# Kernel tuning notes

Measured on AMD Instinct MI355X. Metric: run time of the kernel, lower is better.

## Reference

```python
import jax, jax.numpy as jnp
import numpy as np

B, C, H, W = 4, 192, 128, 128
K = 2048            # selected (changed) tokens per image
HEADS = 3
HD = C // HEADS     # 64
HID = 4 * C         # 768, ConvMlp hidden
N = H * W
EPS = 1e-5


def _layernorm(x, w, b):
    mu = jnp.mean(x, axis=-1, keepdims=True)
    var = jnp.mean((x - mu) ** 2, axis=-1, keepdims=True)
    return (x - mu) / jnp.sqrt(var + EPS) * w + b


def setup_inputs() -> dict:
    key = jax.random.key(0)
    ks = jax.random.split(key, 12)
    x = jax.random.normal(ks[0], (B, C, H, W), dtype=jnp.float32)
    # unique sorted indices per batch (scatter-back must be well defined)
    pkeys = jax.random.split(ks[1], B)
    indices = jnp.sort(
        jax.vmap(lambda k: jax.random.permutation(k, N)[:K])(pkeys), axis=-1
    ).astype(jnp.int64)
    s = 0.02
    return {
        "x": x,
        "indices": indices,
        "ln1_w": jnp.ones((C,), jnp.float32),
        "ln1_b": jnp.zeros((C,), jnp.float32),
        "qkv_w": jax.random.normal(ks[2], (3 * C, C), jnp.float32) * s,
        "proj_w": jax.random.normal(ks[3], (C, C), jnp.float32) * s,
        "proj_b": jnp.zeros((C,), jnp.float32),
        "ln2_w": jnp.ones((C,), jnp.float32),
        "ln2_b": jnp.zeros((C,), jnp.float32),
        "fc1_w": jax.random.normal(ks[4], (HID, C), jnp.float32) * s,
        "fc1_b": jnp.zeros((HID,), jnp.float32),
        "dw_w": jax.random.normal(ks[5], (HID, 1, 3, 3), jnp.float32) * s,  # depthwise OIHW
        "fc2_w": jax.random.normal(ks[6], (C, HID), jnp.float32) * s,
        "fc2_b": jnp.zeros((C,), jnp.float32),
    }


def reference(x, indices, ln1_w, ln1_b, qkv_w, proj_w, proj_b,
              ln2_w, ln2_b, fc1_w, fc1_b, dw_w, fc2_w, fc2_b):
    scale = HD ** (-0.5)
    tokens = x.reshape(B, C, N).transpose(0, 2, 1)          # b n c
    y = _layernorm(tokens, ln1_w, ln1_b)

    # --- masked_attn: gather -> dense MHA on subset -> scatter back ---
    br = jnp.arange(B)[:, None]
    sel = y[br, indices]                                    # b k c
    qkv = sel @ qkv_w.T                                     # b k 3c (no bias)
    qkv = qkv.reshape(B, K, 3, HEADS, HD).transpose(2, 0, 3, 1, 4)
    q, k, v = qkv[0], qkv[1], qkv[2]                        # b h k d
    attn = jax.nn.softmax(jnp.einsum("bhqd,bhkd->bhqk", q, k) * scale, axis=-1)
    out = jnp.einsum("bhqk,bhkd->bhqd", attn, v)            # b h k d
    out = out.transpose(0, 2, 1, 3).reshape(B, K, C) @ proj_w.T + proj_b
    y = y.at[br, indices].set(out)

    tokens = tokens + y                                     # residual adds norm1(x) w/ attn-updated subset
    tokens = _layernorm(tokens, ln2_w, ln2_b)

    # --- ConvMlp: fc1 -> depthwise 3x3 -> GELU -> fc2 ---
    h1 = tokens @ fc1_w.T + fc1_b                           # b n hid
    img = h1.transpose(0, 2, 1).reshape(B, HID, H, W)
    img = jax.lax.conv_general_dilated(
        img, dw_w, (1, 1), "SAME",
        dimension_numbers=("NCHW", "OIHW", "NCHW"),
        feature_group_count=HID)
    h1 = img.reshape(B, HID, N).transpose(0, 2, 1)
    h1 = jax.nn.gelu(h1, approximate=False)
    h2 = h1 @ fc2_w.T + fc2_b

    tokens = tokens + h2
    return tokens.transpose(0, 2, 1).reshape(B, C, H, W)
```

## Files before the change

kernel.cpp:

```cpp
#include <hip/hip_runtime.h>

#define B_ 4
#define C_ 192
#define H_ 128
#define W_ 128
#define N_ (H_*W_)
#define K_ 2048
#define HEADS_ 3
#define HD_ 64
#define HID_ 768
#define NC_ 8
#define KC_ (K_/NC_)

typedef __attribute__((ext_vector_type(4))) float f32x4;
typedef __attribute__((ext_vector_type(8))) short bf16x8;

__device__ __forceinline__ unsigned short f2bf(float f){
  unsigned int u = __float_as_uint(f);
  u += 0x7FFFu + ((u >> 16) & 1u);
  return (unsigned short)(u >> 16);
}
__device__ __forceinline__ float bf2f(unsigned short s){
  return __uint_as_float(((unsigned int)s) << 16);
}
__device__ __forceinline__ unsigned cvtpk(float lo, float hi){
  unsigned r;
  asm("v_cvt_pk_bf16_f32 %0, %1, %2" : "=v"(r) : "v"(lo), "v"(hi));
  return r;
}

__device__ __forceinline__ int load_idx(const unsigned* __restrict__ ip, int pos){
  bool is64 = (ip[1]==0u) & (ip[3]==0u) & (ip[5]==0u) & (ip[7]==0u);
  int v = is64 ? (int)ip[2*pos] : (int)ip[pos];
  return min(max(v, 0), N_-1);
}

__global__ __launch_bounds__(256) void k_ln1(const float* __restrict__ x,
    const float* __restrict__ w, const float* __restrict__ bias,
    unsigned short* __restrict__ y, int b_off){
  int blk = blockIdx.x;
  int bl = blk >> 8;
  int b  = b_off + bl;
  int n0 = (blk & 255) * 64;
  int t  = threadIdx.x;
  int tok = t & 63, q = t >> 6;
  __shared__ float tile[64][C_+1];
  __shared__ float red[8][64];
  __shared__ float wls[C_], bls[C_];
  if (t < C_){ wls[t] = w[t]; bls[t] = bias[t]; }
  const float* xb = x + (size_t)b*C_*N_ + n0;
  float sum = 0.f, sq = 0.f;
#pragma unroll
  for (int i = 0; i < 48; ++i){
    int c = q + 4*i;
    float v = xb[(size_t)c*N_ + tok];
    tile[tok][c] = v;
    sum += v; sq += v*v;
  }
  red[q][tok] = sum; red[4+q][tok] = sq;
  __syncthreads();
  if (q == 0){
    float s  = red[0][tok]+red[1][tok]+red[2][tok]+red[3][tok];
    float s2 = red[4][tok]+red[5][tok]+red[6][tok]+red[7][tok];
    float mu = s*(1.f/C_);
    float rstd = rsqrtf(s2*(1.f/C_) - mu*mu + 1e-5f);
    red[0][tok] = mu; red[1][tok] = rstd;
  }
  __syncthreads();
  unsigned* yb = reinterpret_cast<unsigned*>(y + ((size_t)bl*N_ + n0)*C_);
#pragma unroll
  for (int i = 0; i < 24; ++i){
    int li = t + 256*i;
    int tk = li / 96, c2 = li % 96;
    int c = 2*c2;
    float v0 = (tile[tk][c]  -red[0][tk])*red[1][tk]*wls[c]   + bls[c];
    float v1 = (tile[tk][c+1]-red[0][tk])*red[1][tk]*wls[c+1] + bls[c+1];
    yb[li] = (unsigned)f2bf(v0) | ((unsigned)f2bf(v1) << 16);
  }
}

__global__ __launch_bounds__(256) void k_qkv(const unsigned short* __restrict__ y,
    const unsigned* __restrict__ idx, const float* __restrict__ wq,
    unsigned short* __restrict__ qkv, int b_off){
  const int NT = (3*C_)/64;
  int bid = blockIdx.x;
  int bl  = bid / (16*NT);
  int rem = bid % (16*NT);
  int m0  = (rem / NT) * 128;
  int n0  = (rem % NT) * 64;
  int t = threadIdx.x, lane = t & 63;
  int wv = t >> 6, wm = wv & 1, wn = wv >> 1;
  __shared__ unsigned short Al[128][40];
  __shared__ unsigned short Bl[64][40];
  __shared__ int rows[128];
  if (t < 128) rows[t] = load_idx(idx, (b_off+bl)*K_ + m0 + t);
  __syncthreads();
  f32x4 acc[4][2] = {};
  int l15 = lane & 15, lhi = lane >> 4;
  for (int k0 = 0; k0 < C_; k0 += 32){
    {
      int m = t >> 1;
      const unsigned short* src = y + ((size_t)bl*N_ + rows[m])*C_ + k0;
#pragma unroll
      for (int i = 0; i < 4; ++i){
        int kq = (t & 1) + 2*i;
        *reinterpret_cast<ushort4*>(&Al[m][4*kq]) =
            *reinterpret_cast<const ushort4*>(src + 4*kq);
      }
      int n = t >> 2;
      const float* bsrc = wq + (size_t)(n0+n)*C_ + k0;
#pragma unroll
      for (int i = 0; i < 2; ++i){
        int q = (t & 3) + 4*i;
        float4 v = *reinterpret_cast<const float4*>(bsrc + 4*q);
        ushort4 p; p.x=f2bf(v.x); p.y=f2bf(v.y); p.z=f2bf(v.z); p.w=f2bf(v.w);
        *reinterpret_cast<ushort4*>(&Bl[n][4*q]) = p;
      }
    }
    __syncthreads();
    bf16x8 af[4], bfr[2];
#pragma unroll
    for (int mf = 0; mf < 4; ++mf)
      af[mf] = *reinterpret_cast<const bf16x8*>(&Al[wm*64 + mf*16 + l15][lhi*8]);
#pragma unroll
    for (int nf = 0; nf < 2; ++nf)
      bfr[nf] = *reinterpret_cast<const bf16x8*>(&Bl[wn*32 + nf*16 + l15][lhi*8]);
#pragma unroll
    for (int mf = 0; mf < 4; ++mf)
#pragma unroll
      for (int nf = 0; nf < 2; ++nf)
        acc[mf][nf] = __builtin_amdgcn_mfma_f32_16x16x32_bf16(af[mf], bfr[nf], acc[mf][nf], 0,0,0);
    __syncthreads();
  }
#pragma unroll
  for (int mf = 0; mf < 4; ++mf){
    int mb = m0 + wm*64 + mf*16 + lhi*4;
#pragma unroll
    for (int nf = 0; nf < 2; ++nf){
      int n = n0 + wn*32 + nf*16 + l15;
#pragma unroll
      for (int r = 0; r < 4; ++r)
        qkv[((size_t)bl*K_ + mb + r)*(3*C_) + n] = f2bf(acc[mf][nf][r]);
    }
  }
}

__global__ __launch_bounds__(256) void k_attn(const unsigned short* __restrict__ qkv,
    float* __restrict__ po, float* __restrict__ pml, int nb){
  int bid = blockIdx.x;
  int c   = bid & (NC_-1);
  int qt  = (bid >> 3) & 31;
  int bh  = bid >> 8;
  int h = bh % HEADS_, bl = bh / HEADS_;
  int q0 = qt*64;
  int t = threadIdx.x, lane = t & 63, wv = t >> 6;
  int l15 = lane & 15, lhi = lane >> 4;
  const unsigned short* base = qkv + (size_t)bl*K_*(3*C_) + h*HD_;
  __shared__ unsigned short Ql[64][72];
  __shared__ unsigned short Kl[64][72];
  __shared__ unsigned short Vt[64][72];
  __shared__ unsigned short Pl[4][16][72];
  {
    int r = t >> 2, d0 = (t & 3) * 16;
    const uint4* src = reinterpret_cast<const uint4*>(base + (size_t)(q0+r)*(3*C_) + d0);
    *reinterpret_cast<uint4*>(&Ql[r][d0])   = src[0];
    *reinterpret_cast<uint4*>(&Ql[r][d0+8]) = src[1];
  }
  __syncthreads();
  float m_q = -1e30f, l_q = 0.f;
  f32x4 o[4] = {};
  for (int kt0 = c*KC_; kt0 < c*KC_ + KC_; kt0 += 64){
    {
      int r = t >> 2, d0 = (t & 3) * 16;
      const uint4* src = reinterpret_cast<const uint4*>(base + (size_t)(kt0+r)*(3*C_) + C_ + d0);
      *reinterpret_cast<uint4*>(&Kl[r][d0])   = src[0];
      *reinterpret_cast<uint4*>(&Kl[r][d0+8]) = src[1];
      int kp = t & 31, vd0 = (t >> 5) * 8, k = 2*kp;
      const ushort4* v0 = reinterpret_cast<const ushort4*>(base + (size_t)(kt0+k)*(3*C_)   + 2*C_ + vd0);
      const ushort4* v1 = reinterpret_cast<const ushort4*>(base + (size_t)(kt0+k+1)*(3*C_) + 2*C_ + vd0);
      ushort4 a0 = v0[0], a1 = v0[1], b0 = v1[0], b1 = v1[1];
      unsigned short va[8] = {a0.x,a0.y,a0.z,a0.w,a1.x,a1.y,a1.z,a1.w};
      unsigned short vb[8] = {b0.x,b0.y,b0.z,b0.w,b1.x,b1.y,b1.z,b1.w};
#pragma unroll
      for (int j = 0; j < 8; ++j){
        unsigned u = (unsigned)va[j] | ((unsigned)vb[j] << 16);
        *reinterpret_cast<unsigned*>(&Vt[vd0+j][k]) = u;
      }
    }
    __syncthreads();
    f32x4 s[4] = {};
    __builtin_amdgcn_s_setprio(1);
#pragma unroll
    for (int kt = 0; kt < 2; ++kt){
      bf16x8 qf = *reinterpret_cast<const bf16x8*>(&Ql[wv*16 + l15][kt*32 + lhi*8]);
#pragma unroll
      for (int nt = 0; nt < 4; ++nt){
        bf16x8 kf = *reinterpret_cast<const bf16x8*>(&Kl[nt*16 + l15][kt*32 + lhi*8]);
        s[nt] = __builtin_amdgcn_mfma_f32_16x16x32_bf16(kf, qf, s[nt], 0,0,0);
      }
    }
    __builtin_amdgcn_s_setprio(0);
    float mx = s[0][0];
#pragma unroll
    for (int nt = 0; nt < 4; ++nt)
#pragma unroll
      for (int reg = 0; reg < 4; ++reg) mx = fmaxf(mx, s[nt][reg]);
    mx = fmaxf(mx, __shfl_xor(mx, 16));
    mx = fmaxf(mx, __shfl_xor(mx, 32));
    mx *= 0.125f;
    bool skip = __all(mx <= m_q + 8.f);
    if (!skip){
      float mn = fmaxf(m_q, mx);
      float corr = __expf(m_q - mn);
      l_q *= corr;
      float cr[4];
#pragma unroll
      for (int reg = 0; reg < 4; ++reg) cr[reg] = __shfl(corr, lhi*4 + reg);
#pragma unroll
      for (int nt = 0; nt < 4; ++nt)
#pragma unroll
        for (int reg = 0; reg < 4; ++reg) o[nt][reg] *= cr[reg];
      m_q = mn;
    }
    float ls = 0.f;
#pragma unroll
    for (int nt = 0; nt < 4; ++nt){
      float p0 = __expf(fmaf(s[nt][0], 0.125f, -m_q));
      float p1 = __expf(fmaf(s[nt][1], 0.125f, -m_q));
      float p2 = __expf(fmaf(s[nt][2], 0.125f, -m_q));
      float p3 = __expf(fmaf(s[nt][3], 0.125f, -m_q));
      ls += (p0 + p1) + (p2 + p3);
      uint2 uu;
      uu.x = cvtpk(p0, p1);
      uu.y = cvtpk(p2, p3);
      *reinterpret_cast<uint2*>(&Pl[wv][l15][nt*16 + lhi*4]) = uu;
    }
    ls += __shfl_xor(ls, 16);
    ls += __shfl_xor(ls, 32);
    l_q += ls;
    __threadfence_block();
    __builtin_amdgcn_s_setprio(1);
#pragma unroll
    for (int kt = 0; kt < 2; ++kt){
      bf16x8 pa = *reinterpret_cast<const bf16x8*>(&Pl[wv][l15][kt*32 + lhi*8]);
#pragma unroll
      for (int nt = 0; nt < 4; ++nt){
        bf16x8 vb = *reinterpret_cast<const bf16x8*>(&Vt[nt*16 + l15][kt*32 + lhi*8]);
        o[nt] = __builtin_amdgcn_mfma_f32_16x16x32_bf16(pa, vb, o[nt], 0,0,0);
      }
    }
    __builtin_amdgcn_s_setprio(0);
    __syncthreads();
  }
  int R = nb*HEADS_*K_;
  int rowb = (bl*HEADS_ + h)*K_;
#pragma unroll
  for (int reg = 0; reg < 4; ++reg){
    int rq = rowb + q0 + wv*16 + lhi*4 + reg;
#pragma unroll
    for (int nt = 0; nt < 4; ++nt)
      po[((size_t)c*R + rq)*HD_ + nt*16 + l15] = o[nt][reg];
  }
  if (lhi == 0){
    int rq = rowb + q0 + wv*16 + l15;
    *reinterpret_cast<float2*>(pml + 2*((size_t)c*R + rq)) = make_float2(m_q, l_q);
  }
}

__global__ __launch_bounds__(256) void k_amerge(const float* __restrict__ po,
    const float* __restrict__ pml, unsigned short* __restrict__ ao, int nb){
  int R = nb*HEADS_*K_;
  int row = blockIdx.x*4 + (threadIdx.x >> 6);
  int lane = threadIdx.x & 63;
  float m[NC_], l[NC_];
#pragma unroll
  for (int cc = 0; cc < NC_; ++cc){
    float2 v = *reinterpret_cast<const float2*>(pml + 2*((size_t)cc*R + row));
    m[cc] = v.x; l[cc] = v.y;
  }
  float M = m[0];
#pragma unroll
  for (int cc = 1; cc < NC_; ++cc) M = fmaxf(M, m[cc]);
  float L = 0.f, o = 0.f;
#pragma unroll
  for (int cc = 0; cc < NC_; ++cc){
    float e = __expf(m[cc] - M);
    L += l[cc]*e;
    o += e * po[((size_t)cc*R + row)*HD_ + lane];
  }
  o /= L;
  int q = row & (K_-1);
  int bh = row >> 11;
  int h = bh % HEADS_, bl = bh / HEADS_;
  ao[((size_t)bl*K_ + q)*C_ + h*HD_ + lane] = f2bf(o);
}

__global__ __launch_bounds__(256) void k_proj(const unsigned short* __restrict__ ain,
    const unsigned* __restrict__ idx, const float* __restrict__ pw,
    const float* __restrict__ pb, unsigned short* __restrict__ y, int b_off){
  const int NT = C_/64;
  int bid = blockIdx.x;
  int bl  = bid / (16*NT);
  int rem = bid % (16*NT);
  int m0  = (rem / NT) * 128;
  int n0  = (rem % NT) * 64;
  int t = threadIdx.x, lane = t & 63;
  int wv = t >> 6, wm = wv & 1, wn = wv >> 1;
  __shared__ unsigned short Al[128][40];
  __shared__ unsigned short Bl[64][40];
  __shared__ int rows[128];
  if (t < 128) rows[t] = load_idx(idx, (b_off+bl)*K_ + m0 + t);
  __syncthreads();
  f32x4 acc[4][2] = {};
  int l15 = lane & 15, lhi = lane >> 4;
  for (int k0 = 0; k0 < C_; k0 += 32){
    {
      int m = t >> 1;
      const unsigned short* src = ain + ((size_t)bl*K_ + m0 + m)*C_ + k0;
#pragma unroll
      for (int i = 0; i < 4; ++i){
        int kq = (t & 1) + 2*i;
        *reinterpret_cast<ushort4*>(&Al[m][4*kq]) =
            *reinterpret_cast<const ushort4*>(src + 4*kq);
      }
      int n = t >> 2;
      const float* bsrc = pw + (size_t)(n0+n)*C_ + k0;
#pragma unroll
      for (int i = 0; i < 2; ++i){
        int q = (t & 3) + 4*i;
        float4 v = *reinterpret_cast<const float4*>(bsrc + 4*q);
        ushort4 p; p.x=f2bf(v.x); p.y=f2bf(v.y); p.z=f2bf(v.z); p.w=f2bf(v.w);
        *reinterpret_cast<ushort4*>(&Bl[n][4*q]) = p;
      }
    }
    __syncthreads();
    bf16x8 af[4], bfr[2];
#pragma unroll
    for (int mf = 0; mf < 4; ++mf)
      af[mf] = *reinterpret_cast<const bf16x8*>(&Al[wm*64 + mf*16 + l15][lhi*8]);
#pragma unroll
    for (int nf = 0; nf < 2; ++nf)
      bfr[nf] = *reinterpret_cast<const bf16x8*>(&Bl[wn*32 + nf*16 + l15][lhi*8]);
#pragma unroll
    for (int mf = 0; mf < 4; ++mf)
#pragma unroll
      for (int nf = 0; nf < 2; ++nf)
        acc[mf][nf] = __builtin_amdgcn_mfma_f32_16x16x32_bf16(af[mf], bfr[nf], acc[mf][nf], 0,0,0);
    __syncthreads();
  }
#pragma unroll
  for (int mf = 0; mf < 4; ++mf){
    int mb = wm*64 + mf*16 + lhi*4;
#pragma unroll
    for (int nf = 0; nf < 2; ++nf){
      int n = n0 + wn*32 + nf*16 + l15;
      float bv = pb[n];
#pragma unroll
      for (int r = 0; r < 4; ++r)
        y[((size_t)bl*N_ + rows[mb + r])*C_ + n] = f2bf(acc[mf][nf][r] + bv);
    }
  }
}

__global__ __launch_bounds__(256) void k_ln2(const float* __restrict__ x,
    const unsigned short* __restrict__ y, const float* __restrict__ w,
    const float* __restrict__ bias, float* __restrict__ ln2t, int b_off){
  int blk = blockIdx.x;
  int bl = blk >> 8;
  int b  = b_off + bl;
  int n0 = (blk & 255) * 64;
  int t  = threadIdx.x;
  int tok = t & 63, q = t >> 6;
  __shared__ float tile[64][C_+1];
  __shared__ float red[8][64];
  __shared__ float wls[C_], bls[C_];
  if (t < C_){ wls[t] = w[t]; bls[t] = bias[t]; }
  const unsigned* yb = reinterpret_cast<const unsigned*>(y + ((size_t)bl*N_ + n0)*C_);
#pragma unroll
  for (int i = 0; i < 24; ++i){
    int li = t + 256*i;
    unsigned u = yb[li];
    int tk = li / 96, c2 = li % 96;
    tile[tk][2*c2]   = bf2f((unsigned short)(u & 0xffffu));
    tile[tk][2*c2+1] = bf2f((unsigned short)(u >> 16));
  }
  __syncthreads();
  const float* xb = x + (size_t)b*C_*N_ + n0;
  float sum = 0.f, sq = 0.f;
#pragma unroll
  for (int i = 0; i < 48; ++i){
    int c = q + 4*i;
    float v = xb[(size_t)c*N_ + tok] + tile[tok][c];
    tile[tok][c] = v;
    sum += v; sq += v*v;
  }
  red[q][tok] = sum; red[4+q][tok] = sq;
  __syncthreads();
  if (q == 0){
    float s  = red[0][tok]+red[1][tok]+red[2][tok]+red[3][tok];
    float s2 = red[4][tok]+red[5][tok]+red[6][tok]+red[7][tok];
    float mu = s*(1.f/C_);
    float rstd = rsqrtf(s2*(1.f/C_) - mu*mu + 1e-5f);
    red[0][tok] = mu; red[1][tok] = rstd;
  }
  __syncthreads();
  float* ob = ln2t + (size_t)b*C_*N_ + n0;
  float mu = red[0][tok], rstd = red[1][tok];
#pragma unroll
  for (int i = 0; i < 48; ++i){
    int c = q + 4*i;
    ob[(size_t)c*N_ + tok] = (tile[tok][c]-mu)*rstd*wls[c] + bls[c];
  }
}

__global__ __launch_bounds__(256) void k_fc1(const float* __restrict__ ln2t,
    const float* __restrict__ wgt, const float* __restrict__ bias,
    unsigned short* __restrict__ h1, int b_off){
  int bid = blockIdx.x;
  int bl  = bid >> 8;
  int rem = bid & 255;
  int m0  = (rem >> 1) * 128;
  int nh  = (rem & 1) * 6;
  int t = threadIdx.x, lane = t & 63;
  int wv = t >> 6, wm = wv & 1, wn = wv >> 1;
  int l15 = lane & 15, lhi = lane >> 4;
  __shared__ unsigned short Al[128][200];
  __shared__ unsigned short Bl[64][200];
  const float* a = ln2t + (size_t)(b_off+bl)*C_*N_ + m0;
  unsigned short* hb = h1 + (size_t)bl*HID_*N_;
  {
    int m = t & 127, half = t >> 7;
#pragma unroll
    for (int i = 0; i < 48; ++i){
      int p = half + 2*i;
      float v0 = a[(size_t)(2*p)*N_ + m];
      float v1 = a[(size_t)(2*p+1)*N_ + m];
      unsigned u = (unsigned)f2bf(v0) | ((unsigned)f2bf(v1) << 16);
      *reinterpret_cast<unsigned*>(&Al[m][2*p]) = u;
    }
  }
  for (int nt = 0; nt < 6; ++nt){
    int n0 = (nh + nt)*64;
    __syncthreads();
    {
      int n = t >> 2;
      const float* bsrc = wgt + (size_t)(n0+n)*C_;
#pragma unroll
      for (int i = 0; i < 12; ++i){
        int q = (t & 3) + 4*i;
        float4 v = *reinterpret_cast<const float4*>(bsrc + 4*q);
        ushort4 p; p.x=f2bf(v.x); p.y=f2bf(v.y); p.z=f2bf(v.z); p.w=f2bf(v.w);
        *reinterpret_cast<ushort4*>(&Bl[n][4*q]) = p;
      }
    }
    __syncthreads();
    f32x4 acc[4][2] = {};
#pragma unroll
    for (int ks = 0; ks < 6; ++ks){
      bf16x8 af[4], bfr[2];
#pragma unroll
      for (int mf = 0; mf < 4; ++mf)
        af[mf] = *reinterpret_cast<const bf16x8*>(&Al[wm*64 + mf*16 + l15][ks*32 + lhi*8]);
#pragma unroll
      for (int nf = 0; nf < 2; ++nf)
        bfr[nf] = *reinterpret_cast<const bf16x8*>(&Bl[wn*32 + nf*16 + l15][ks*32 + lhi*8]);
#pragma unroll
      for (int mf = 0; mf < 4; ++mf)
#pragma unroll
        for (int nf = 0; nf < 2; ++nf)
          acc[mf][nf] = __builtin_amdgcn_mfma_f32_16x16x32_bf16(af[mf], bfr[nf], acc[mf][nf], 0,0,0);
    }
#pragma unroll
    for (int mf = 0; mf < 4; ++mf){
      int mb = m0 + wm*64 + mf*16 + lhi*4;
#pragma unroll
      for (int nf = 0; nf < 2; ++nf){
        int n = n0 + wn*32 + nf*16 + l15;
        float bv = bias[n];
        ushort4 pk;
        pk.x = f2bf(acc[mf][nf][0] + bv);
        pk.y = f2bf(acc[mf][nf][1] + bv);
        pk.z = f2bf(acc[mf][nf][2] + bv);
        pk.w = f2bf(acc[mf][nf][3] + bv);
        *reinterpret_cast<ushort4*>(&hb[(size_t)n*N_ + mb]) = pk;
      }
    }
  }
}

__global__ __launch_bounds__(512) void k_fc2f(const unsigned short* __restrict__ h1,
    const float* __restrict__ dw, const float* __restrict__ wgt,
    const float* __restrict__ bias, float* __restrict__ out, int b_off){
  int nwg = gridDim.x;
  int cpx = nwg >> 3;
  int bid = (blockIdx.x & 7)*cpx + (blockIdx.x >> 3);
  int bl  = bid >> 7;
  int r   = bid & 127;
  int b   = b_off + bl;
  int t = threadIdx.x, lane = t & 63, wv = t >> 6;
  int wm = wv & 1, wn = wv >> 1;
  int l15 = lane & 15, lhi = lane >> 4;
  __shared__ unsigned short Ht[32][3][136];
  __shared__ unsigned short Alc[128][40];
  __shared__ unsigned short Bl[192][40];
  __shared__ float Dwl[288];
  const unsigned short* h1b = h1 + (size_t)bl*HID_*N_;
  f32x4 acc[4][3] = {};
  int cch = t & 31, j0 = (t >> 5) * 8;
  for (int k0 = 0; k0 < HID_; k0 += 32){
    __syncthreads();
#pragma unroll
    for (int i = 0; i < 3; ++i){
      int li = t + 512*i;
      int ch = li / 48, rem = li % 48, dy = rem >> 4, seg = rem & 15;
      int rr = r - 1 + dy;
      uint4 v = make_uint4(0u,0u,0u,0u);
      if (rr >= 0 && rr < H_)
        v = *reinterpret_cast<const uint4*>(h1b + (size_t)(k0+ch)*N_ + rr*W_ + seg*8);
      *reinterpret_cast<uint4*>(&Ht[ch][dy][seg*8]) = v;
    }
#pragma unroll
    for (int i = 0; i < 3; ++i){
      int li = t + 512*i;
      int row = li >> 3, seg = li & 7;
      float4 v = *reinterpret_cast<const float4*>(wgt + (size_t)row*HID_ + k0 + seg*4);
      ushort4 p; p.x=f2bf(v.x); p.y=f2bf(v.y); p.z=f2bf(v.z); p.w=f2bf(v.w);
      *reinterpret_cast<ushort4*>(&Bl[row][seg*4]) = p;
    }
    if (t < 288) Dwl[t] = dw[k0*9 + t];
    __syncthreads();
    {
      const float* wp = &Dwl[cch*9];
      float s[8] = {0.f,0.f,0.f,0.f,0.f,0.f,0.f,0.f};
#pragma unroll
      for (int dy = 0; dy < 3; ++dy){
        const unsigned short* rp = &Ht[cch][dy][j0];
        bf16x8 mid = *reinterpret_cast<const bf16x8*>(rp);
        float v[10];
        v[0] = (j0 > 0)   ? bf2f(rp[-1]) : 0.f;
        v[9] = (j0 < 120) ? bf2f(rp[8])  : 0.f;
#pragma unroll
        for (int j = 0; j < 8; ++j) v[1+j] = bf2f((unsigned short)mid[j]);
        float wa = wp[3*dy], wb = wp[3*dy+1], wc = wp[3*dy+2];
#pragma unroll
        for (int j = 0; j < 8; ++j)
          s[j] += v[j]*wa + v[j+1]*wb + v[j+2]*wc;
      }
#pragma unroll
      for (int j = 0; j < 8; ++j){
        float xx = s[j];
        Alc[j0+j][cch] = f2bf(0.5f*xx*(1.f + erff(xx*0.70710678f)));
      }
    }
    __syncthreads();
    bf16x8 af[4], bfr[3];
#pragma unroll
    for (int mf = 0; mf < 4; ++mf)
      af[mf] = *reinterpret_cast<const bf16x8*>(&Alc[wm*64 + mf*16 + l15][lhi*8]);
#pragma unroll
    for (int nf = 0; nf < 3; ++nf)
      bfr[nf] = *reinterpret_cast<const bf16x8*>(&Bl[wn*48 + nf*16 + l15][lhi*8]);
    __builtin_amdgcn_s_setprio(1);
#pragma unroll
    for (int mf = 0; mf < 4; ++mf)
#pragma unroll
      for (int nf = 0; nf < 3; ++nf)
        acc[mf][nf] = __builtin_amdgcn_mfma_f32_16x16x32_bf16(af[mf], bfr[nf], acc[mf][nf], 0,0,0);
    __builtin_amdgcn_s_setprio(0);
  }
#pragma unroll
  for (int mf = 0; mf < 4; ++mf){
    int tok = r*W_ + wm*64 + mf*16 + lhi*4;
#pragma unroll
    for (int nf = 0; nf < 3; ++nf){
      int oc = wn*48 + nf*16 + l15;
      float bv = bias[oc];
      size_t off = ((size_t)b*C_ + oc)*N_ + tok;
      float4 rr = *reinterpret_cast<const float4*>(out + off);
      float4 v = make_float4(rr.x + acc[mf][nf][0] + bv, rr.y + acc[mf][nf][1] + bv,
                             rr.z + acc[mf][nf][2] + bv, rr.w + acc[mf][nf][3] + bv);
      *reinterpret_cast<float4*>(out + off) = v;
    }
  }
}

extern "C" void kernel_launch(void* const* d_in, const int* in_sizes, int n_in,
                              void* d_out, int out_size, void* d_ws, size_t ws_size,
                              hipStream_t stream) {
  const float*    x      = (const float*)d_in[0];
  const unsigned* idx    = (const unsigned*)d_in[1];
  const float*    ln1_w  = (const float*)d_in[2];
  const float*    ln1_b  = (const float*)d_in[3];
  const float*    qkv_w  = (const float*)d_in[4];
  const float*    proj_w = (const float*)d_in[5];
  const float*    proj_b = (const float*)d_in[6];
  const float*    ln2_w  = (const float*)d_in[7];
  const float*    ln2_b  = (const float*)d_in[8];
  const float*    fc1_w  = (const float*)d_in[9];
  const float*    fc1_b  = (const float*)d_in[10];
  const float*    dw_w   = (const float*)d_in[11];
  const float*    fc2_w  = (const float*)d_in[12];
  const float*    fc2_b  = (const float*)d_in[13];
  float* out = (float*)d_out;

  const size_t SZY = (size_t)N_*C_*2;
  const size_t SZQ = (size_t)K_*3*C_*2;
  const size_t SZA = (size_t)K_*C_*2;
  const size_t SZO = (size_t)NC_*HEADS_*K_*HD_*4;
  const size_t SZH = (size_t)HID_*N_*2;
  int nb = (ws_size >= (size_t)B_*SZH) ? B_ : 1;

  char* ws = (char*)d_ws;
  unsigned short* y16  = (unsigned short*)ws;
  unsigned short* qkvb = (unsigned short*)(ws + (size_t)nb*SZY);
  unsigned short* aob  = (unsigned short*)(ws + (size_t)nb*(SZY+SZQ));
  float*          po   = (float*)(ws + (size_t)nb*(SZY+SZQ+SZA));
  float*          pml  = (float*)(ws + (size_t)nb*(SZY+SZQ+SZA+SZO));
  unsigned short* h1s  = (unsigned short*)ws;

  for (int b0 = 0; b0 < B_; b0 += nb){
    k_ln1   <<<nb*256,             256, 0, stream>>>(x, ln1_w, ln1_b, y16, b0);
    k_qkv   <<<nb*16*9,            256, 0, stream>>>(y16, idx, qkv_w, qkvb, b0);
    k_attn  <<<nb*HEADS_*32*NC_,   256, 0, stream>>>(qkvb, po, pml, nb);
    k_amerge<<<nb*HEADS_*K_/4,     256, 0, stream>>>(po, pml, aob, nb);
    k_proj  <<<nb*16*3,            256, 0, stream>>>(aob, idx, proj_w, proj_b, y16, b0);
    k_ln2   <<<nb*256,             256, 0, stream>>>(x, y16, ln2_w, ln2_b, out, b0);
    k_fc1   <<<nb*256,             256, 0, stream>>>(out, fc1_w, fc1_b, h1s, b0);
    k_fc2f  <<<nb*128,             512, 0, stream>>>(h1s, dw_w, fc2_w, fc2_b, out, b0);
  }
}
```

Before: 269.8 us.

## Split fc2 tiles into half-row blocks and use tanh GELU approximation

The fused depthwise-conv/GELU/fc2 kernel now handles half an image row (64 tokens) per workgroup instead of a full row. This doubles the grid and raises occupancy, and the shared-memory tile is reorganised with halo columns. The exact erf GELU is replaced with a tanh-based approximation built on __expf to cut transcendental cost. The trade-offs are more redundant halo loads, fc2 weight tiles loaded twice as often, and a small numerical deviation from exact GELU.

```diff
diff --git a/kernel.cpp b/kernel.cpp
--- a/kernel.cpp
+++ b/kernel.cpp
@@ -27,6 +27,13 @@
   unsigned r;
   asm("v_cvt_pk_bf16_f32 %0, %1, %2" : "=v"(r) : "v"(lo), "v"(hi));
   return r;
+}
+__device__ __forceinline__ float gelu_fast(float x){
+  float y = 0.7978845608f*x*(1.f + 0.044715f*x*x);
+  float e = __expf(2.f*fabsf(y));
+  float t = 1.f - 2.f/(1.f + e);
+  t = copysignf(t, y);
+  return 0.5f*x*(1.f + t);
 }
 
 __device__ __forceinline__ int load_idx(const unsigned* __restrict__ ip, int pos){
@@ -494,30 +501,35 @@
   int nwg = gridDim.x;
   int cpx = nwg >> 3;
   int bid = (blockIdx.x & 7)*cpx + (blockIdx.x >> 3);
-  int bl  = bid >> 7;
-  int r   = bid & 127;
+  int bl  = bid >> 8;
+  int rem = bid & 255;
+  int r    = rem >> 1;
+  int c0   = (rem & 1) * 64;
   int b   = b_off + bl;
   int t = threadIdx.x, lane = t & 63, wv = t >> 6;
   int wm = wv & 1, wn = wv >> 1;
   int l15 = lane & 15, lhi = lane >> 4;
-  __shared__ unsigned short Ht[32][3][136];
-  __shared__ unsigned short Alc[128][40];
+  __shared__ unsigned short Ht[3][32][88];
+  __shared__ unsigned short Alc[64][48];
   __shared__ unsigned short Bl[192][40];
   __shared__ float Dwl[288];
   const unsigned short* h1b = h1 + (size_t)bl*HID_*N_;
-  f32x4 acc[4][3] = {};
-  int cch = t & 31, j0 = (t >> 5) * 8;
+  f32x4 acc[2][3] = {};
+  int cch = t & 31, grp = t >> 5;
   for (int k0 = 0; k0 < HID_; k0 += 32){
     __syncthreads();
 #pragma unroll
-    for (int i = 0; i < 3; ++i){
+    for (int i = 0; i < 2; ++i){
       int li = t + 512*i;
-      int ch = li / 48, rem = li % 48, dy = rem >> 4, seg = rem & 15;
-      int rr = r - 1 + dy;
-      uint4 v = make_uint4(0u,0u,0u,0u);
-      if (rr >= 0 && rr < H_)
-        v = *reinterpret_cast<const uint4*>(h1b + (size_t)(k0+ch)*N_ + rr*W_ + seg*8);
-      *reinterpret_cast<uint4*>(&Ht[ch][dy][seg*8]) = v;
+      if (li < 960){
+        int ch = li / 30, rem2 = li % 30, dy = rem2 / 10, s = rem2 % 10;
+        int rr = r - 1 + dy;
+        int colst = c0 - 8 + 8*s;
+        uint4 v = make_uint4(0u,0u,0u,0u);
+        if (rr >= 0 && rr < H_ && colst >= 0 && colst < W_)
+          v = *reinterpret_cast<const uint4*>(h1b + (size_t)(k0+ch)*N_ + rr*W_ + colst);
+        *reinterpret_cast<uint4*>(&Ht[dy][ch][8*s]) = v;
+      }
     }
 #pragma unroll
     for (int i = 0; i < 3; ++i){
@@ -531,46 +543,45 @@
     __syncthreads();
     {
       const float* wp = &Dwl[cch*9];
-      float s[8] = {0.f,0.f,0.f,0.f,0.f,0.f,0.f,0.f};
+      float s4[4] = {0.f,0.f,0.f,0.f};
 #pragma unroll
       for (int dy = 0; dy < 3; ++dy){
-        const unsigned short* rp = &Ht[cch][dy][j0];
-        bf16x8 mid = *reinterpret_cast<const bf16x8*>(rp);
-        float v[10];
-        v[0] = (j0 > 0)   ? bf2f(rp[-1]) : 0.f;
-        v[9] = (j0 < 120) ? bf2f(rp[8])  : 0.f;
-#pragma unroll
-        for (int j = 0; j < 8; ++j) v[1+j] = bf2f((unsigned short)mid[j]);
+        const unsigned* hp = reinterpret_cast<const unsigned*>(&Ht[dy][cch][0]);
+        int base = (6 + 4*grp) >> 1;
+        unsigned u0 = hp[base], u1 = hp[base+1], u2 = hp[base+2], u3 = hp[base+3];
+        float v[8];
+        v[0] = bf2f((unsigned short)(u0 & 0xffffu)); v[1] = bf2f((unsigned short)(u0 >> 16));
+        v[2] = bf2f((unsigned short)(u1 & 0xffffu)); v[3] = bf2f((unsigned short)(u1 >> 16));
+        v[4] = bf2f((unsigned short)(u2 & 0xffffu)); v[5] = bf2f((unsigned short)(u2 >> 16));
+        v[6] = bf2f((unsigned short)(u3 & 0xffffu)); v[7] = bf2f((unsigned short)(u3 >> 16));
         float wa = wp[3*dy], wb = wp[3*dy+1], wc = wp[3*dy+2];
 #pragma unroll
-        for (int j = 0; j < 8; ++j)
-          s[j] += v[j]*wa + v[j+1]*wb + v[j+2]*wc;
-      }
-#pragma unroll
-      for (int j = 0; j < 8; ++j){
-        float xx = s[j];
-        Alc[j0+j][cch] = f2bf(0.5f*xx*(1.f + erff(xx*0.70710678f)));
-      }
-    }
-    __syncthreads();
-    bf16x8 af[4], bfr[3];
-#pragma unroll
-    for (int mf = 0; mf < 4; ++mf)
-      af[mf] = *reinterpret_cast<const bf16x8*>(&Alc[wm*64 + mf*16 + l15][lhi*8]);
+        for (int j = 0; j < 4; ++j)
+          s4[j] += v[1+j]*wa + v[2+j]*wb + v[3+j]*wc;
+      }
+#pragma unroll
+      for (int j = 0; j < 4; ++j)
+        Alc[grp*4 + j][cch] = f2bf(gelu_fast(s4[j]));
+    }
+    __syncthreads();
+    bf16x8 af[2], bfr[3];
+#pragma unroll
+    for (int mf = 0; mf < 2; ++mf)
+      af[mf] = *reinterpret_cast<const bf16x8*>(&Alc[wm*32 + mf*16 + l15][lhi*8]);
 #pragma unroll
     for (int nf = 0; nf < 3; ++nf)
       bfr[nf] = *reinterpret_cast<const bf16x8*>(&Bl[wn*48 + nf*16 + l15][lhi*8]);
     __builtin_amdgcn_s_setprio(1);
 #pragma unroll
-    for (int mf = 0; mf < 4; ++mf)
+    for (int mf = 0; mf < 2; ++mf)
 #pragma unroll
       for (int nf = 0; nf < 3; ++nf)
         acc[mf][nf] = __builtin_amdgcn_mfma_f32_16x16x32_bf16(af[mf], bfr[nf], acc[mf][nf], 0,0,0);
     __builtin_amdgcn_s_setprio(0);
   }
 #pragma unroll
-  for (int mf = 0; mf < 4; ++mf){
-    int tok = r*W_ + wm*64 + mf*16 + lhi*4;
+  for (int mf = 0; mf < 2; ++mf){
+    int tok = r*W_ + c0 + wm*32 + mf*16 + lhi*4;
 #pragma unroll
     for (int nf = 0; nf < 3; ++nf){
       int oc = wn*48 + nf*16 + l15;
@@ -626,6 +637,6 @@
     k_proj  <<<nb*16*3,            256, 0, stream>>>(aob, idx, proj_w, proj_b, y16, b0);
     k_ln2   <<<nb*256,             256, 0, stream>>>(x, y16, ln2_w, ln2_b, out, b0);
     k_fc1   <<<nb*256,             256, 0, stream>>>(out, fc1_w, fc1_b, h1s, b0);
-    k_fc2f  <<<nb*128,             512, 0, stream>>>(h1s, dw_w, fc2_w, fc2_b, out, b0);
-  }
-}
+    k_fc2f  <<<nb*256,             512, 0, stream>>>(h1s, dw_w, fc2_w, fc2_b, out, b0);
+  }
+}
```

Result: slower. 319.8 us (+18.5%).

## Double-buffer h1 halo tiles in fc2 kernel and use tanh-approximate GELU

Applied to the files above, without the earlier changes.

In the fused depthwise+GELU+fc2 kernel, the next K-chunk of h1 rows is prefetched into registers while the current chunk is processed, then written to a second LDS buffer after the conv stage. This is meant to hide global load latency behind the convolution and MFMA work. The exact erf GELU is also replaced by a tanh approximation built on __expf, which lowers the ALU cost but departs from the reference's exact GELU. Leftover unused variables remain in the code.

```diff
diff --git a/kernel.cpp b/kernel.cpp
--- a/kernel.cpp
+++ b/kernel.cpp
@@ -27,6 +27,13 @@
   unsigned r;
   asm("v_cvt_pk_bf16_f32 %0, %1, %2" : "=v"(r) : "v"(lo), "v"(hi));
   return r;
+}
+__device__ __forceinline__ float gelu_fast(float x){
+  float y = 0.7978845608f*x*(1.f + 0.044715f*x*x);
+  float e = __expf(2.f*fabsf(y));
+  float t = 1.f - 2.f/(1.f + e);
+  t = copysignf(t, y);
+  return 0.5f*x*(1.f + t);
 }
 
 __device__ __forceinline__ int load_idx(const unsigned* __restrict__ ip, int pos){
@@ -500,15 +507,20 @@
   int t = threadIdx.x, lane = t & 63, wv = t >> 6;
   int wm = wv & 1, wn = wv >> 1;
   int l15 = lane & 15, lhi = lane >> 4;
-  __shared__ unsigned short Ht[32][3][136];
+  __shared__ unsigned short Ht[2][32][3][136];
   __shared__ unsigned short Alc[128][40];
   __shared__ unsigned short Bl[192][40];
   __shared__ float Dwl[288];
   const unsigned short* h1b = h1 + (size_t)bl*HID_*N_;
   f32x4 acc[4][3] = {};
   int cch = t & 31, j0 = (t >> 5) * 8;
-  for (int k0 = 0; k0 < HID_; k0 += 32){
-    __syncthreads();
+  int s_ch, s_dy, s_seg, s_rr;
+  {
+    int li = t;
+    (void)li;
+  }
+  uint4 hr[3];
+  auto hload = [&](int k0n){
 #pragma unroll
     for (int i = 0; i < 3; ++i){
       int li = t + 512*i;
@@ -516,9 +528,23 @@
       int rr = r - 1 + dy;
       uint4 v = make_uint4(0u,0u,0u,0u);
       if (rr >= 0 && rr < H_)
-        v = *reinterpret_cast<const uint4*>(h1b + (size_t)(k0+ch)*N_ + rr*W_ + seg*8);
-      *reinterpret_cast<uint4*>(&Ht[ch][dy][seg*8]) = v;
-    }
+        v = *reinterpret_cast<const uint4*>(h1b + (size_t)(k0n+ch)*N_ + rr*W_ + seg*8);
+      hr[i] = v;
+    }
+  };
+  auto hwrite = [&](int buf){
+#pragma unroll
+    for (int i = 0; i < 3; ++i){
+      int li = t + 512*i;
+      int ch = li / 48, rem = li % 48, dy = rem >> 4, seg = rem & 15;
+      *reinterpret_cast<uint4*>(&Ht[buf][ch][dy][seg*8]) = hr[i];
+    }
+  };
+  (void)s_ch; (void)s_dy; (void)s_seg; (void)s_rr;
+  hload(0); hwrite(0);
+  for (int c24 = 0; c24 < 24; ++c24){
+    int k0 = c24*32, cur = c24 & 1;
+    __syncthreads();
 #pragma unroll
     for (int i = 0; i < 3; ++i){
       int li = t + 512*i;
@@ -528,13 +554,14 @@
       *reinterpret_cast<ushort4*>(&Bl[row][seg*4]) = p;
     }
     if (t < 288) Dwl[t] = dw[k0*9 + t];
-    __syncthreads();
+    if (c24 < 23) hload(k0 + 32);
     {
       const float* wp = &Dwl[cch*9];
       float s[8] = {0.f,0.f,0.f,0.f,0.f,0.f,0.f,0.f};
+      __syncthreads();
 #pragma unroll
       for (int dy = 0; dy < 3; ++dy){
-        const unsigned short* rp = &Ht[cch][dy][j0];
+        const unsigned short* rp = &Ht[cur][cch][dy][j0];
         bf16x8 mid = *reinterpret_cast<const bf16x8*>(rp);
         float v[10];
         v[0] = (j0 > 0)   ? bf2f(rp[-1]) : 0.f;
@@ -547,12 +574,11 @@
           s[j] += v[j]*wa + v[j+1]*wb + v[j+2]*wc;
       }
 #pragma unroll
-      for (int j = 0; j < 8; ++j){
-        float xx = s[j];
-        Alc[j0+j][cch] = f2bf(0.5f*xx*(1.f + erff(xx*0.70710678f)));
-      }
-    }
-    __syncthreads();
+      for (int j = 0; j < 8; ++j)
+        Alc[j0+j][cch] = f2bf(gelu_fast(s[j]));
+    }
+    __syncthreads();
+    if (c24 < 23) hwrite(cur ^ 1);
     bf16x8 af[4], bfr[3];
 #pragma unroll
     for (int mf = 0; mf < 4; ++mf)
```

Result: no change. 268.9 us (-0.4%).

## Read depthwise halo directly from global, prefetch fc2 weights, use tanh GELU

Applied to the files above, without the earlier changes.

In the fused depthwise-conv + GELU + fc2 kernel, the shared-memory staging of the 3-row halo tile and the depthwise weights is removed. Each thread now reads its h1 rows and conv weights straight from global memory, which drops one barrier per K-step. The fc2 weight tile for the next step is register-prefetched so its load overlaps the current step's compute. Exact erf GELU is replaced by the tanh approximation via exp, which is cheaper but deviates slightly from the reference's exact GELU and adds redundant, less coalesced global reads.

```diff
diff --git a/kernel.cpp b/kernel.cpp
--- a/kernel.cpp
+++ b/kernel.cpp
@@ -27,6 +27,13 @@
   unsigned r;
   asm("v_cvt_pk_bf16_f32 %0, %1, %2" : "=v"(r) : "v"(lo), "v"(hi));
   return r;
+}
+__device__ __forceinline__ float gelu_fast(float x){
+  float y = 0.7978845608f*x*(1.f + 0.044715f*x*x);
+  float e = __expf(2.f*fabsf(y));
+  float t = 1.f - 2.f/(1.f + e);
+  t = copysignf(t, y);
+  return 0.5f*x*(1.f + t);
 }
 
 __device__ __forceinline__ int load_idx(const unsigned* __restrict__ ip, int pos){
@@ -500,41 +507,42 @@
   int t = threadIdx.x, lane = t & 63, wv = t >> 6;
   int wm = wv & 1, wn = wv >> 1;
   int l15 = lane & 15, lhi = lane >> 4;
-  __shared__ unsigned short Ht[32][3][136];
   __shared__ unsigned short Alc[128][40];
   __shared__ unsigned short Bl[192][40];
-  __shared__ float Dwl[288];
   const unsigned short* h1b = h1 + (size_t)bl*HID_*N_;
   f32x4 acc[4][3] = {};
   int cch = t & 31, j0 = (t >> 5) * 8;
-  for (int k0 = 0; k0 < HID_; k0 += 32){
-    __syncthreads();
-#pragma unroll
-    for (int i = 0; i < 3; ++i){
-      int li = t + 512*i;
-      int ch = li / 48, rem = li % 48, dy = rem >> 4, seg = rem & 15;
-      int rr = r - 1 + dy;
-      uint4 v = make_uint4(0u,0u,0u,0u);
-      if (rr >= 0 && rr < H_)
-        v = *reinterpret_cast<const uint4*>(h1b + (size_t)(k0+ch)*N_ + rr*W_ + seg*8);
-      *reinterpret_cast<uint4*>(&Ht[ch][dy][seg*8]) = v;
-    }
+  float4 wreg[3];
+  auto wload = [&](int k0n){
 #pragma unroll
     for (int i = 0; i < 3; ++i){
       int li = t + 512*i;
       int row = li >> 3, seg = li & 7;
-      float4 v = *reinterpret_cast<const float4*>(wgt + (size_t)row*HID_ + k0 + seg*4);
+      wreg[i] = *reinterpret_cast<const float4*>(wgt + (size_t)row*HID_ + k0n + seg*4);
+    }
+  };
+  wload(0);
+  for (int c24 = 0; c24 < 24; ++c24){
+    int k0 = c24*32;
+    __syncthreads();
+#pragma unroll
+    for (int i = 0; i < 3; ++i){
+      int li = t + 512*i;
+      int row = li >> 3, seg = li & 7;
+      float4 v = wreg[i];
       ushort4 p; p.x=f2bf(v.x); p.y=f2bf(v.y); p.z=f2bf(v.z); p.w=f2bf(v.w);
       *reinterpret_cast<ushort4*>(&Bl[row][seg*4]) = p;
     }
-    if (t < 288) Dwl[t] = dw[k0*9 + t];
-    __syncthreads();
+    if (c24 < 23) wload(k0 + 32);
     {
-      const float* wp = &Dwl[cch*9];
+      const unsigned short* plane = h1b + (size_t)(k0+cch)*N_;
+      const float* wp = dw + (size_t)(k0+cch)*9;
       float s[8] = {0.f,0.f,0.f,0.f,0.f,0.f,0.f,0.f};
 #pragma unroll
       for (int dy = 0; dy < 3; ++dy){
-        const unsigned short* rp = &Ht[cch][dy][j0];
+        int rr = r - 1 + dy;
+        if (rr < 0 || rr >= H_) continue;
+        const unsigned short* rp = plane + rr*W_ + j0;
         bf16x8 mid = *reinterpret_cast<const bf16x8*>(rp);
         float v[10];
         v[0] = (j0 > 0)   ? bf2f(rp[-1]) : 0.f;
@@ -547,10 +555,8 @@
           s[j] += v[j]*wa + v[j+1]*wb + v[j+2]*wc;
       }
 #pragma unroll
-      for (int j = 0; j < 8; ++j){
-        float xx = s[j];
-        Alc[j0+j][cch] = f2bf(0.5f*xx*(1.f + erff(xx*0.70710678f)));
-      }
+      for (int j = 0; j < 8; ++j)
+        Alc[j0+j][cch] = f2bf(gelu_fast(s[j]));
     }
     __syncthreads();
     bf16x8 af[4], bfr[3];
```

After: 326.4 us. +21.0%, slower.
